# Kernel optimization log

Measured on AMD Instinct MI355X. Metric: run time of the kernel, lower is better.

The kernel has to match this reference:

```python
import jax, jax.numpy as jnp
import numpy as np

N = 48          # nagents
D = 16          # ndims
K = 2           # edge_type (excluding type-0 'no edge')
H = 256         # MLP hidden units
B = 32          # batch
PRED = 8        # pred_steps


def setup_inputs() -> dict:
    key = jax.random.key(0)
    ks = jax.random.split(key, 12)
    # fully-connected edges without self loops (fc_matrix)
    src_np, tgt_np = np.nonzero(np.ones((N, N), np.int8) - np.eye(N, dtype=np.int8))
    src_idx = jnp.asarray(src_np, jnp.int32)   # [E]
    tgt_idx = jnp.asarray(tgt_np, jnp.int32)   # [E]
    E = src_idx.shape[0]                       # 2256

    time_segs = jax.random.normal(ks[0], (B, 1, N, D), jnp.float32)
    types = jax.random.randint(ks[1], (B, E), 0, K + 1)
    edge_types = jax.nn.one_hot(types, K + 1, dtype=jnp.float32)  # [B,E,K+1]

    def glorot(k, shape, fan_in):
        return jax.random.normal(k, shape, jnp.float32) * (1.0 / np.sqrt(fan_in))

    enc_W1 = glorot(ks[2], (K, 2 * D, H), 2 * D)
    enc_b1 = jnp.zeros((K, H), jnp.float32)
    enc_W2 = glorot(ks[3], (K, H, H), H)
    enc_b2 = jnp.zeros((K, H), jnp.float32)
    dec_W1 = glorot(ks[4], (D + H, H), D + H)
    dec_b1 = jnp.zeros((H,), jnp.float32)
    dec_W2 = glorot(ks[5], (H, H), H)
    dec_b2 = jnp.zeros((H,), jnp.float32)
    out_W = glorot(ks[6], (H, D), H)
    out_b = jnp.zeros((D,), jnp.float32)

    return dict(time_segs=time_segs, edge_types=edge_types,
                src_idx=src_idx, tgt_idx=tgt_idx,
                enc_W1=enc_W1, enc_b1=enc_b1, enc_W2=enc_W2, enc_b2=enc_b2,
                dec_W1=dec_W1, dec_b1=dec_b1, dec_W2=dec_W2, dec_b2=dec_b2,
                out_W=out_W, out_b=out_b)


def reference(time_segs, edge_types, src_idx, tgt_idx,
              enc_W1, enc_b1, enc_W2, enc_b2,
              dec_W1, dec_b1, dec_W2, dec_b2,
              out_W, out_b):
    # time_segs: [B, 1, N, D]; edge_types: [B, E, K+1]
    b = time_segs.shape[0]
    # transpose to [B, N, T, D]; time_seg_len == 1 so conv1d is identity and
    # each step consumes only the latest state.
    state = jnp.transpose(time_segs, (0, 2, 1, 3))[:, :, -1, :]  # [B, N, D]
    et = edge_types[:, :, 1:, None]                              # [B, E, K, 1]

    outs = []
    for _ in range(PRED):
        # gather node pairs -> per-edge message [B, E, 2D]
        edge_msg = jnp.concatenate([state[:, src_idx], state[:, tgt_idx]], axis=-1)
        # per-edge-type MLP encode: [B, E, K, H]
        h = jax.nn.relu(jnp.einsum('bef,kfh->bekh', edge_msg, enc_W1) + enc_b1)
        h = jax.nn.relu(jnp.einsum('bekh,khg->bekg', h, enc_W2) + enc_b2)
        # masked reduce over edge types -> [B, E, H]
        agg = jnp.sum(h * et, axis=2)
        # scatter-aggregate edge messages to target nodes -> [B, N, H]
        node_msg = jnp.zeros((b, N, H), agg.dtype).at[:, tgt_idx].add(agg)
        # node decode
        node_in = jnp.concatenate([state, node_msg], axis=-1)    # [B, N, D+H]
        d = jax.nn.relu(node_in @ dec_W1 + dec_b1)
        d = jax.nn.relu(d @ dec_W2 + dec_b2)
        # residual update
        state = state + d @ out_W + out_b                        # [B, N, D]
        outs.append(state)
    return jnp.stack(outs, axis=1)  # [B, PRED, N, D]
```

## Files before the change

kernel.cpp:

```cpp
#include <hip/hip_runtime.h>

#define NN    48
#define DD    16
#define HH    256
#define EE    2256
#define BB    32
#define NPRED 8
#define LSTR  56
#define PQS   1040
#define TMAX  7
#define ROWB  80
#define APL   (TMAX*16*ROWB)

typedef __attribute__((ext_vector_type(4))) float f32x4;
typedef __attribute__((ext_vector_type(8))) short short8;

__device__ __forceinline__ float bf2f(unsigned short h) {
    union { unsigned u; float f; } v; v.u = ((unsigned)h) << 16; return v.f;
}
__device__ __forceinline__ unsigned short f2bf(float x) {
    union { float f; unsigned u; } v; v.f = x;
    unsigned r = v.u + 0x7fffu + ((v.u >> 16) & 1u);
    return (unsigned short)(r >> 16);
}
__device__ __forceinline__ unsigned perm_hi16(unsigned xB, unsigned xA, unsigned sel) {
    unsigned d;
    asm("v_perm_b32 %0, %1, %2, %3" : "=v"(d) : "v"(xB), "v"(xA), "s"(sel));
    return d;
}
struct Split3 { unsigned d0, d1, d2; };
__device__ __forceinline__ Split3 split2(float u0, float u1, unsigned sel)
{
    union F { float f; unsigned u; };
    Split3 o;
    F x0, x1; x0.f = u0; x1.f = u1;
    o.d0 = perm_hi16(x1.u, x0.u, sel);
    F h0a, h0b; h0a.u = x0.u & 0xffff0000u; h0b.u = x1.u & 0xffff0000u;
    F e0a, e0b; e0a.f = u0 - h0a.f; e0b.f = u1 - h0b.f;
    o.d1 = perm_hi16(e0b.u, e0a.u, sel);
    F h1a, h1b; h1a.u = e0a.u & 0xffff0000u; h1b.u = e0b.u & 0xffff0000u;
    F e1a, e1b; e1a.f = e0a.f - h1a.f; e1b.f = e0b.f - h1b.f;
    o.d2 = perm_hi16(e1b.u, e1a.u, sel);
    return o;
}
union PackA { unsigned u[4]; short8 s; };

__global__ __launch_bounds__(256) void k_setup(
    const float* __restrict__ time_segs,
    const float* __restrict__ edge_types,
    const float* __restrict__ W1,
    const float* __restrict__ W2,
    const float* __restrict__ b1,
    float* __restrict__ state,
    float* __restrict__ W1T,
    unsigned short* __restrict__ W2f,
    float* __restrict__ PQ,
    int* __restrict__ lists,
    int* __restrict__ counts)
{
    const int tid = blockIdx.x * 256 + threadIdx.x;
    const int NT = 384*256;
    for (int i = tid; i < BB*NN*DD; i += NT)
        state[i] = time_segs[i];
    for (int i = tid; i < 2*HH*32; i += NT) {
        const int t = i >> 13, r = i & 8191, h = r >> 5, f = r & 31;
        W1T[i] = W1[(t*32 + f)*HH + h];
    }
    for (int i = tid; i < 2*8*16*64*8; i += NT) {
        const int j  = i & 7, l = (i >> 3) & 63, nt = (i >> 9) & 15;
        const int kt = (i >> 13) & 7, t = (i >> 16) & 1;
        const int k = kt*32 + ((l >> 4) << 3) + j;
        const int n = nt*16 + (l & 15);
        const float w = W2[((size_t)t*HH + k)*HH + n];
        const unsigned short h0 = f2bf(w);  const float r1 = w  - bf2f(h0);
        const unsigned short h1 = f2bf(r1); const float r2 = r1 - bf2f(h1);
        const unsigned short h2 = f2bf(r2);
        const size_t rest = (size_t)kt*8192 + nt*512 + l*8 + j;
        W2f[(size_t)(t*3+0)*65536 + rest] = h0;
        W2f[(size_t)(t*3+1)*65536 + rest] = h1;
        W2f[(size_t)(t*3+2)*65536 + rest] = h2;
    }
    for (int i = tid; i < BB*NN*1024; i += NT) {
        const int c  = i & 255;
        const int pq = (i >> 8) & 1;
        const int t  = (i >> 9) & 1;
        const int nb = i >> 10;
        float v = pq ? b1[t*HH + c] : 0.f;
        #pragma unroll
        for (int f = 0; f < DD; ++f)
            v = fmaf(time_segs[nb*DD + f], W1[(t*32 + pq*16 + f)*HH + c], v);
        PQ[(size_t)nb*PQS + (i & 1023)] = v;
    }
    if (tid < BB*NN) {
        const int b = tid / NN;
        const int n = tid % NN;
        int* lst = lists + tid * LSTR;
        int c = 0;
        for (int s = 0; s < NN; ++s) {
            if (s == n) continue;
            const int e = s * 47 + (n > s ? n - 1 : n);
            if (edge_types[((size_t)b*EE + e)*3 + 1] > 0.5f) lst[c++] = s;
        }
        const int c1 = c;
        for (int s = 0; s < NN; ++s) {
            if (s == n) continue;
            const int e = s * 47 + (n > s ? n - 1 : n);
            if (edge_types[((size_t)b*EE + e)*3 + 2] > 0.5f) lst[c++] = s;
        }
        counts[tid*2 + 0] = c1;
        counts[tid*2 + 1] = c - c1;
        for (int i = c; i < LSTR; ++i) lst[i] = 0;
    }
}

#define MFMA6(Ax, Bi, a)                                                       \
    a = __builtin_amdgcn_mfma_f32_16x16x32_bf16(Ax[2], Bi[0], a, 0, 0, 0);     \
    a = __builtin_amdgcn_mfma_f32_16x16x32_bf16(Ax[1], Bi[1], a, 0, 0, 0);     \
    a = __builtin_amdgcn_mfma_f32_16x16x32_bf16(Ax[0], Bi[2], a, 0, 0, 0);     \
    a = __builtin_amdgcn_mfma_f32_16x16x32_bf16(Ax[1], Bi[0], a, 0, 0, 0);     \
    a = __builtin_amdgcn_mfma_f32_16x16x32_bf16(Ax[0], Bi[1], a, 0, 0, 0);     \
    a = __builtin_amdgcn_mfma_f32_16x16x32_bf16(Ax[0], Bi[0], a, 0, 0, 0);

#define MM1(qq)                                                                \
    {                                                                          \
        short8 Af[3];                                                          \
        const char* ap = Apl + (qq)*16*ROWB + abase;                           \
        _Pragma("unroll")                                                      \
        for (int p = 0; p < 3; ++p) Af[p] = *(const short8*)(ap + p*APL);      \
        f32x4 x0 = acc[qq][0], x1 = acc[qq][1];                                \
        MFMA6(Af, Bf[0], x0)                                                   \
        MFMA6(Af, Bf[1], x1)                                                   \
        acc[qq][0] = x0; acc[qq][1] = x1;                                      \
    }

__global__ __launch_bounds__(512, 4) void k_enc(
    const int*   __restrict__ lists,
    const int*   __restrict__ counts,
    const float* __restrict__ PQ,
    const unsigned short* __restrict__ W2f,
    const float* __restrict__ b2,
    float* __restrict__ node_msg)
{
    const int lb   = (blockIdx.x & 7)*96 + (blockIdx.x >> 3);
    const int b    = lb / 24;
    const int pair = lb % 24;
    const int n0   = pair * 2;
    const int tid  = threadIdx.x;
    const int lane = tid & 63, wave = tid >> 6;
    const unsigned PSEL = 0x07060302u;

    __shared__ __align__(16) char Apl[3*APL];
    __shared__ int rowinfo_s[TMAX*16];

    const int c00 = counts[(b*NN + n0    )*2 + 0];
    const int c10 = counts[(b*NN + n0    )*2 + 1];
    const int c01 = counts[(b*NN + n0 + 1)*2 + 0];
    const int c11 = counts[(b*NN + n0 + 1)*2 + 1];
    const int tA  = c00 + c01, tB = c10 + c11;
    const int tAt = (tA + 15) >> 4, tBt = (tB + 15) >> 4;
    const int tiles = tAt + tBt;
    const int rows  = tiles*16;

    if (tid < TMAX*16) {
        const int r = tid;
        int g = 4, src = 0;
        if (r < tAt*16) {
            if (r < c00)     { src = lists[(b*NN + n0    )*LSTR + r];        g = 0; }
            else if (r < tA) { src = lists[(b*NN + n0 + 1)*LSTR + (r - c00)]; g = 1; }
        } else if (r < rows) {
            const int s = r - tAt*16;
            if (s < c10)     { src = lists[(b*NN + n0    )*LSTR + c00 + s];        g = 2; }
            else if (s < tB) { src = lists[(b*NN + n0 + 1)*LSTR + c01 + (s - c10)]; g = 3; }
        }
        rowinfo_s[r] = src | (g << 8);
    }
    __syncthreads();

    f32x4 acc[TMAX][2];
    #pragma unroll
    for (int q = 0; q < TMAX; ++q) {
        acc[q][0] = (f32x4){0.f, 0.f, 0.f, 0.f};
        acc[q][1] = (f32x4){0.f, 0.f, 0.f, 0.f};
    }

    const float* PQb = PQ + (size_t)b*NN*PQS;
    const int ntb  = wave*2;
    const int abase = (lane & 15)*ROWB + (lane >> 4)*16;

    #pragma unroll 1
    for (int kt = 0; kt < 8; ++kt) {
        {
            const int row  = tid >> 2, quad = tid & 3;
            if (row < rows) {
                const int info = rowinfo_s[row];
                const int src  = info & 255;
                const int nd   = (info >> 8) & 1;
                const int tq   = (row >= tAt*16) ? 1 : 0;
                const int cols = kt*32 + quad*8;
                const float* pr = PQb + src*PQS      + tq*512 +       cols;
                const float* qr = PQb + (n0+nd)*PQS  + tq*512 + 256 + cols;
                const float4 Pa = *(const float4*)pr, Pb = *(const float4*)(pr+4);
                const float4 Qa = *(const float4*)qr, Qb = *(const float4*)(qr+4);
                const float u0 = fmaxf(Pa.x + Qa.x, 0.f);
                const float u1 = fmaxf(Pa.y + Qa.y, 0.f);
                const float u2 = fmaxf(Pa.z + Qa.z, 0.f);
                const float u3 = fmaxf(Pa.w + Qa.w, 0.f);
                const float u4 = fmaxf(Pb.x + Qb.x, 0.f);
                const float u5 = fmaxf(Pb.y + Qb.y, 0.f);
                const float u6 = fmaxf(Pb.z + Qb.z, 0.f);
                const float u7 = fmaxf(Pb.w + Qb.w, 0.f);
                const Split3 s0 = split2(u0, u1, PSEL);
                const Split3 s1 = split2(u2, u3, PSEL);
                const Split3 s2 = split2(u4, u5, PSEL);
                const Split3 s3 = split2(u6, u7, PSEL);
                char* w = Apl + row*ROWB + quad*16;
                PackA A0, A1, A2;
                A0.u[0]=s0.d0; A0.u[1]=s1.d0; A0.u[2]=s2.d0; A0.u[3]=s3.d0;
                A1.u[0]=s0.d1; A1.u[1]=s1.d1; A1.u[2]=s2.d1; A1.u[3]=s3.d1;
                A2.u[0]=s0.d2; A2.u[1]=s1.d2; A2.u[2]=s2.d2; A2.u[3]=s3.d2;
                *(short8*)(w)         = A0.s;
                *(short8*)(w + APL)   = A1.s;
                *(short8*)(w + 2*APL) = A2.s;
            }
        }
        __syncthreads();

        #pragma unroll
        for (int sec = 0; sec < 2; ++sec) {
            const int qlo = sec ? tAt : 0;
            const int qhi = sec ? tiles : tAt;
            if (qlo >= qhi) continue;
            short8 Bf[2][3];
            #pragma unroll
            for (int i = 0; i < 2; ++i)
                #pragma unroll
                for (int p = 0; p < 3; ++p)
                    Bf[i][p] = *(const short8*)(W2f + ((size_t)(sec*3+p)*65536
                                 + (size_t)kt*8192 + (size_t)(ntb + i)*512 + (size_t)lane*8));
            #pragma unroll
            for (int q = 0; q < TMAX; ++q) {
                if (q >= qlo && q < qhi) { MM1(q) }
            }
        }
        __syncthreads();
    }

    float b2v[2][2];
    #pragma unroll
    for (int t = 0; t < 2; ++t)
        #pragma unroll
        for (int i = 0; i < 2; ++i)
            b2v[t][i] = b2[t*HH + (ntb + i)*16 + (lane & 15)];

    float p0[2], p1[2];
    p0[0] = p0[1] = p1[0] = p1[1] = 0.f;
    #pragma unroll
    for (int q = 0; q < TMAX; ++q) {
        if (q < tiles) {
            const bool secB = (q >= tAt);
            int gv[4];
            #pragma unroll
            for (int rr = 0; rr < 4; ++rr)
                gv[rr] = rowinfo_s[q*16 + (lane >> 4)*4 + rr] >> 8;
            #pragma unroll
            for (int i = 0; i < 2; ++i) {
                const float bias = secB ? b2v[1][i] : b2v[0][i];
                #pragma unroll
                for (int rr = 0; rr < 4; ++rr) {
                    const float v = fmaxf(acc[q][i][rr] + bias, 0.f);
                    const bool valid = gv[rr] < 4;
                    p0[i] += (valid && !(gv[rr] & 1)) ? v : 0.f;
                    p1[i] += (valid &&  (gv[rr] & 1)) ? v : 0.f;
                }
            }
        }
    }
    #pragma unroll
    for (int i = 0; i < 2; ++i) {
        float v0 = p0[i], v1 = p1[i];
        v0 += __shfl_xor(v0, 16); v0 += __shfl_xor(v0, 32);
        v1 += __shfl_xor(v1, 16); v1 += __shfl_xor(v1, 32);
        if ((lane >> 4) == 0) {
            node_msg[((size_t)(b*NN + n0  ))*HH + (ntb + i)*16 + lane] = v0;
            node_msg[((size_t)(b*NN + n0+1))*HH + (ntb + i)*16 + lane] = v1;
        }
    }
}

__global__ __launch_bounds__(256, 2) void k_dec(
    float* __restrict__ state,
    const float* __restrict__ nm,
    const float* __restrict__ W1, const float* __restrict__ b1,
    const float* __restrict__ W2, const float* __restrict__ b2,
    const float* __restrict__ W3, const float* __restrict__ b3,
    const float* __restrict__ eW1T,
    const float* __restrict__ eb1,
    float* __restrict__ PQ,
    float* __restrict__ out, int step)
{
    const int lb   = (blockIdx.x & 7)*32 + (blockIdx.x >> 3);
    const int b    = lb / 8;
    const int row0 = (lb % 8) * 6;
    const int c    = threadIdx.x;

    __shared__ float in_s[6][272];
    __shared__ float d1s[6][HH];
    __shared__ float stn[6][DD];

    for (int i = c; i < 6*272; i += 256) {
        const int m = i / 272, k = i % 272;
        const int r = row0 + m;
        in_s[m][k] = (k < DD)
            ? state[((size_t)b*NN + r)*DD + k]
            : nm[((size_t)b*NN + r)*HH + (k - DD)];
    }
    __syncthreads();

    float a0[6];
    {
        const float bb = b1[c];
        #pragma unroll
        for (int m = 0; m < 6; ++m) a0[m] = bb;
        #pragma unroll 2
        for (int k4 = 0; k4 < 68; ++k4) {
            const float* wr = W1 + (k4*4)*HH;
            const float w0=wr[c], w1_=wr[HH+c], w2_=wr[2*HH+c], w3=wr[3*HH+c];
            #pragma unroll
            for (int m = 0; m < 6; ++m) {
                const float4 h = *(const float4*)&in_s[m][k4*4];
                a0[m] = fmaf(h.x,w0, fmaf(h.y,w1_, fmaf(h.z,w2_, fmaf(h.w,w3, a0[m]))));
            }
        }
        #pragma unroll
        for (int m = 0; m < 6; ++m) d1s[m][c] = fmaxf(a0[m], 0.f);
    }
    __syncthreads();
    {
        const float bb = b2[c];
        #pragma unroll
        for (int m = 0; m < 6; ++m) a0[m] = bb;
        #pragma unroll 2
        for (int k4 = 0; k4 < 64; ++k4) {
            const float* wr = W2 + (k4*4)*HH;
            const float w0=wr[c], w1_=wr[HH+c], w2_=wr[2*HH+c], w3=wr[3*HH+c];
            #pragma unroll
            for (int m = 0; m < 6; ++m) {
                const float4 h = *(const float4*)&d1s[m][k4*4];
                a0[m] = fmaf(h.x,w0, fmaf(h.y,w1_, fmaf(h.z,w2_, fmaf(h.w,w3, a0[m]))));
            }
        }
        __syncthreads();
        #pragma unroll
        for (int m = 0; m < 6; ++m) in_s[m][c] = fmaxf(a0[m], 0.f);
    }
    __syncthreads();
    if (c < 96) {
        const int m = c >> 4, cc = c & 15;
        float a = b3[cc];
        #pragma unroll 4
        for (int k4 = 0; k4 < 64; ++k4) {
            const float4 h = *(const float4*)&in_s[m][k4*4];
            a += h.x*W3[(k4*4+0)*16+cc] + h.y*W3[(k4*4+1)*16+cc]
               + h.z*W3[(k4*4+2)*16+cc] + h.w*W3[(k4*4+3)*16+cc];
        }
        const int r = row0 + m;
        const float v = state[((size_t)b*NN + r)*DD + cc] + a;
        state[((size_t)b*NN + r)*DD + cc] = v;
        out[(((size_t)b*NPRED + step)*NN + r)*DD + cc] = v;
        stn[m][cc] = v;
    }
    __syncthreads();
    float4 sm[6][4];
    #pragma unroll
    for (int m = 0; m < 6; ++m)
        #pragma unroll
        for (int f4 = 0; f4 < 4; ++f4)
            sm[m][f4] = *(const float4*)&stn[m][f4*4];
    #pragma unroll
    for (int k = 0; k < 4; ++k) {
        const int combo = c + 256*k;
        const int cc = combo & 255;
        const int pq = (combo >> 8) & 1;
        const int t  = combo >> 9;
        const float* wc = eW1T + ((size_t)t*HH + cc)*32 + pq*16;
        float4 w[4];
        #pragma unroll
        for (int f4 = 0; f4 < 4; ++f4) w[f4] = ((const float4*)wc)[f4];
        const float bias = pq ? eb1[t*HH + cc] : 0.f;
        #pragma unroll
        for (int m = 0; m < 6; ++m) {
            float v = bias;
            #pragma unroll
            for (int f4 = 0; f4 < 4; ++f4) {
                const float4 s = sm[m][f4];
                v = fmaf(s.x,w[f4].x, fmaf(s.y,w[f4].y, fmaf(s.z,w[f4].z, fmaf(s.w,w[f4].w, v))));
            }
            PQ[(size_t)(b*NN + row0 + m)*PQS + t*512 + pq*256 + cc] = v;
        }
    }
}

extern "C" void kernel_launch(void* const* d_in, const int* in_sizes, int n_in,
                              void* d_out, int out_size, void* d_ws, size_t ws_size,
                              hipStream_t stream)
{
    const float* time_segs  = (const float*)d_in[0];
    const float* edge_types = (const float*)d_in[1];
    const float* enc_W1 = (const float*)d_in[4];
    const float* enc_b1 = (const float*)d_in[5];
    const float* enc_W2 = (const float*)d_in[6];
    const float* enc_b2 = (const float*)d_in[7];
    const float* dec_W1 = (const float*)d_in[8];
    const float* dec_b1 = (const float*)d_in[9];
    const float* dec_W2 = (const float*)d_in[10];
    const float* dec_b2 = (const float*)d_in[11];
    const float* out_W  = (const float*)d_in[12];
    const float* out_b  = (const float*)d_in[13];
    float* out = (float*)d_out;

    float* state    = (float*)d_ws;
    float* node_msg = state + BB*NN*DD;
    float* W1T      = node_msg + BB*NN*HH;
    unsigned short* W2f = (unsigned short*)(W1T + 2*HH*32);
    int*   lists    = (int*)(W2f + 2*3*65536);
    int*   counts   = lists + BB*NN*LSTR;
    float* PQ       = (float*)(counts + BB*NN*2);

    k_setup<<<384, 256, 0, stream>>>(time_segs, edge_types, enc_W1, enc_W2,
                                     enc_b1, state, W1T, W2f, PQ, lists, counts);
    for (int stp = 0; stp < NPRED; ++stp) {
        k_enc<<<BB*24, 512, 0, stream>>>(lists, counts, PQ, W2f,
                                         enc_b2, node_msg);
        k_dec<<<BB*8, 256, 0, stream>>>(state, node_msg,
                                        dec_W1, dec_b1, dec_W2, dec_b2,
                                        out_W, out_b, W1T, enc_b1, PQ, out, stp);
    }
}
```

Baseline: 594.5 us.

## Double-buffer encoder A-tile in LDS to overlap build with MFMA

Splits the shared-memory A-operand tile into two buffers. The next k-step's tile is built (global PQ loads, add+ReLU, bf16 split packing) into one buffer while MFMAs consume the other, which removes one barrier per iteration. Per-thread row offsets are hoisted out of the loop. LDS use doubles to about 53 KB per block, which may cut how many 512-thread blocks fit on a CU below the launch-bounds target of 4.

```diff
diff --git a/kernel.cpp b/kernel.cpp
--- a/kernel.cpp
+++ b/kernel.cpp
@@ -11,6 +11,7 @@
 #define TMAX  7
 #define ROWB  80
 #define APL   (TMAX*16*ROWB)
+#define ABUF  (3*APL)
 
 typedef __attribute__((ext_vector_type(4))) float f32x4;
 typedef __attribute__((ext_vector_type(8))) short short8;
@@ -124,7 +125,7 @@
 #define MM1(qq)                                                                \
     {                                                                          \
         short8 Af[3];                                                          \
-        const char* ap = Apl + (qq)*16*ROWB + abase;                           \
+        const char* ap = bufc + (qq)*16*ROWB + abase;                          \
         _Pragma("unroll")                                                      \
         for (int p = 0; p < 3; ++p) Af[p] = *(const short8*)(ap + p*APL);      \
         f32x4 x0 = acc[qq][0], x1 = acc[qq][1];                                \
@@ -149,7 +150,7 @@
     const int lane = tid & 63, wave = tid >> 6;
     const unsigned PSEL = 0x07060302u;
 
-    __shared__ __align__(16) char Apl[3*APL];
+    __shared__ __align__(16) char Apl[2*ABUF];
     __shared__ int rowinfo_s[TMAX*16];
 
     const int c00 = counts[(b*NN + n0    )*2 + 0];
@@ -176,6 +177,19 @@
     }
     __syncthreads();
 
+    const int brow  = tid >> 2, bquad = tid & 3;
+    int bpoff = 0, bqoff = 0;
+    bool bact = false;
+    if (brow < rows) {
+        const int info = rowinfo_s[brow];
+        const int src  = info & 255;
+        const int nd   = (info >> 8) & 1;
+        const int tq   = (brow >= tAt*16) ? 1 : 0;
+        bpoff = src*PQS      + tq*512 +       bquad*8;
+        bqoff = (n0+nd)*PQS  + tq*512 + 256 + bquad*8;
+        bact = true;
+    }
+
     f32x4 acc[TMAX][2];
     #pragma unroll
     for (int q = 0; q < TMAX; ++q) {
@@ -187,44 +201,43 @@
     const int ntb  = wave*2;
     const int abase = (lane & 15)*ROWB + (lane >> 4)*16;
 
+    auto build = [&](int kt, char* buf) {
+        if (bact) {
+            const float* pr = PQb + bpoff + kt*32;
+            const float* qr = PQb + bqoff + kt*32;
+            const float4 Pa = *(const float4*)pr, Pb = *(const float4*)(pr+4);
+            const float4 Qa = *(const float4*)qr, Qb = *(const float4*)(qr+4);
+            const float u0 = fmaxf(Pa.x + Qa.x, 0.f);
+            const float u1 = fmaxf(Pa.y + Qa.y, 0.f);
+            const float u2 = fmaxf(Pa.z + Qa.z, 0.f);
+            const float u3 = fmaxf(Pa.w + Qa.w, 0.f);
+            const float u4 = fmaxf(Pb.x + Qb.x, 0.f);
+            const float u5 = fmaxf(Pb.y + Qb.y, 0.f);
+            const float u6 = fmaxf(Pb.z + Qb.z, 0.f);
+            const float u7 = fmaxf(Pb.w + Qb.w, 0.f);
+            const Split3 s0 = split2(u0, u1, PSEL);
+            const Split3 s1 = split2(u2, u3, PSEL);
+            const Split3 s2 = split2(u4, u5, PSEL);
+            const Split3 s3 = split2(u6, u7, PSEL);
+            char* w = buf + brow*ROWB + bquad*16;
+            PackA A0, A1, A2;
+            A0.u[0]=s0.d0; A0.u[1]=s1.d0; A0.u[2]=s2.d0; A0.u[3]=s3.d0;
+            A1.u[0]=s0.d1; A1.u[1]=s1.d1; A1.u[2]=s2.d1; A1.u[3]=s3.d1;
+            A2.u[0]=s0.d2; A2.u[1]=s1.d2; A2.u[2]=s2.d2; A2.u[3]=s3.d2;
+            *(short8*)(w)         = A0.s;
+            *(short8*)(w + APL)   = A1.s;
+            *(short8*)(w + 2*APL) = A2.s;
+        }
+    };
+
+    build(0, Apl);
+    __syncthreads();
+
     #pragma unroll 1
     for (int kt = 0; kt < 8; ++kt) {
-        {
-            const int row  = tid >> 2, quad = tid & 3;
-            if (row < rows) {
-                const int info = rowinfo_s[row];
-                const int src  = info & 255;
-                const int nd   = (info >> 8) & 1;
-                const int tq   = (row >= tAt*16) ? 1 : 0;
-                const int cols = kt*32 + quad*8;
-                const float* pr = PQb + src*PQS      + tq*512 +       cols;
-                const float* qr = PQb + (n0+nd)*PQS  + tq*512 + 256 + cols;
-                const float4 Pa = *(const float4*)pr, Pb = *(const float4*)(pr+4);
-                const float4 Qa = *(const float4*)qr, Qb = *(const float4*)(qr+4);
-                const float u0 = fmaxf(Pa.x + Qa.x, 0.f);
-                const float u1 = fmaxf(Pa.y + Qa.y, 0.f);
-                const float u2 = fmaxf(Pa.z + Qa.z, 0.f);
-                const float u3 = fmaxf(Pa.w + Qa.w, 0.f);
-                const float u4 = fmaxf(Pb.x + Qb.x, 0.f);
-                const float u5 = fmaxf(Pb.y + Qb.y, 0.f);
-                const float u6 = fmaxf(Pb.z + Qb.z, 0.f);
-                const float u7 = fmaxf(Pb.w + Qb.w, 0.f);
-                const Split3 s0 = split2(u0, u1, PSEL);
-                const Split3 s1 = split2(u2, u3, PSEL);
-                const Split3 s2 = split2(u4, u5, PSEL);
-                const Split3 s3 = split2(u6, u7, PSEL);
-                char* w = Apl + row*ROWB + quad*16;
-                PackA A0, A1, A2;
-                A0.u[0]=s0.d0; A0.u[1]=s1.d0; A0.u[2]=s2.d0; A0.u[3]=s3.d0;
-                A1.u[0]=s0.d1; A1.u[1]=s1.d1; A1.u[2]=s2.d1; A1.u[3]=s3.d1;
-                A2.u[0]=s0.d2; A2.u[1]=s1.d2; A2.u[2]=s2.d2; A2.u[3]=s3.d2;
-                *(short8*)(w)         = A0.s;
-                *(short8*)(w + APL)   = A1.s;
-                *(short8*)(w + 2*APL) = A2.s;
-            }
-        }
-        __syncthreads();
-
+        const int cur = kt & 1;
+        const char* bufc = Apl + cur*ABUF;
+        if (kt < 7) build(kt+1, Apl + (cur^1)*ABUF);
         #pragma unroll
         for (int sec = 0; sec < 2; ++sec) {
             const int qlo = sec ? tAt : 0;
```

New measurement: 571.4 us. 3.9% less time.
